# Optimization experiments

Hardware: AMD Instinct MI355X
Metric: run time of the kernel (lower is better)

## Reference

```python
import jax, jax.numpy as jnp
import numpy as np

V, D = 100000, 300
B, NCTX, NNEG = 16384, 10, 20


def setup_inputs() -> dict:
    key = jax.random.key(0)
    k1, k2, k3, k4, k5 = jax.random.split(key, 5)
    bound = 0.5 / D
    in_embed_w = jax.random.uniform(k1, (V, D), jnp.float32, -bound, bound)
    # torch init is zeros for out_embed; use small random values so the
    # negative-sampling math is numerically non-trivial for testing.
    out_embed_w = jax.random.normal(k2, (V, D), jnp.float32) * 0.01
    context_words = jax.random.randint(k3, (B, NCTX), 0, V)
    center_word = jax.random.randint(k4, (B,), 0, V)
    neg_words = jax.random.randint(k5, (B, NNEG), 0, V)
    return {
        "context_words": context_words,
        "center_word": center_word,
        "neg_words": neg_words,
        "in_embed_w": in_embed_w,
        "out_embed_w": out_embed_w,
    }


def reference(context_words, center_word, neg_words, in_embed_w, out_embed_w):
    # gather + mean-pool context embeddings: [B, 2w, D] -> [B, D]
    ctx_mean = jnp.mean(in_embed_w[context_words], axis=1)
    # positive score: dot(ctx_mean, out_embed[center])  -> [B]
    pos_emb = out_embed_w[center_word]                      # [B, D]
    pos_score = jnp.sum(ctx_mean * pos_emb, axis=1)         # [B]
    # negative scores: bmm([B, K, D], [B, D, 1]) -> [B, K]
    neg_emb = out_embed_w[neg_words]                        # [B, K, D]
    neg_score = jnp.einsum('bkd,bd->bk', neg_emb, ctx_mean)  # [B, K]
    loss = -jnp.mean(
        jax.nn.log_sigmoid(pos_score)
        + jnp.sum(jax.nn.log_sigmoid(-neg_score), axis=1)
    )
    return loss
```

## Files before the change

### kernel.cpp

```cpp
#include <hip/hip_runtime.h>
#include <math.h>

#define DIM    300
#define CH     75
#define NCTX   10
#define NNEG   20
#define NROWS  (1 + NNEG)
#define BLOCK  256
#define G      7

__device__ __forceinline__ float log_sigmoid(float x) {
    return fminf(x, 0.0f) - log1pf(expf(-fabsf(x)));
}
__device__ __forceinline__ float dot4(float4 a, float4 b) {
    return a.x * b.x + a.y * b.y + a.z * b.z + a.w * b.w;
}
__device__ __forceinline__ float4 add4(float4 a, float4 b) {
    return make_float4(a.x + b.x, a.y + b.y, a.z + b.z, a.w + b.w);
}

__global__ __launch_bounds__(BLOCK) void cbow_loss_kernel(
    const int*   __restrict__ ctx,
    const int*   __restrict__ center,
    const int*   __restrict__ neg,
    const float* __restrict__ in_w,
    const float* __restrict__ out_w,
    float*       __restrict__ out,
    int B, float inv_b)
{
    __shared__ float wsum[4];

    const int tid  = threadIdx.x;
    const int wave = tid >> 6;
    const int lane = tid & 63;
    const int b    = blockIdx.x * 4 + wave;

    float loss = 0.f;
    if (b < B) {
        int myidx = 0;
        if (lane < NCTX)                 myidx = ctx[b * NCTX + lane];
        else if (lane == NCTX)           myidx = center[b];
        else if (lane < NCTX + NROWS)    myidx = neg[b * NNEG + (lane - NCTX - 1)];

        const int   c1 = lane;
        const int   c2 = (64 + lane < CH) ? 64 + lane : CH - 1;
        const float w1 = (64 + lane < CH) ? 1.f : 0.f;

        float4 a0 = make_float4(0.f, 0.f, 0.f, 0.f);
        float4 a1 = make_float4(0.f, 0.f, 0.f, 0.f);
        #pragma unroll
        for (int j = 0; j < NCTX; ++j) {
            const int w = __shfl(myidx, j, 64);
            const float4* row = (const float4*)(in_w + (long long)w * DIM);
            a0 = add4(a0, row[c1]);
            a1 = add4(a1, row[c2]);
        }
        const float s0 = 1.f / NCTX;
        const float s1 = w1 / NCTX;
        const float4 m0 = make_float4(a0.x * s0, a0.y * s0, a0.z * s0, a0.w * s0);
        const float4 m1 = make_float4(a1.x * s1, a1.y * s1, a1.z * s1, a1.w * s1);

        #pragma unroll
        for (int t = 0; t < 3; ++t) {
            float4 r0[G], r1[G];
            #pragma unroll
            for (int k = 0; k < G; ++k) {
                const int w = __shfl(myidx, NCTX + t * G + k, 64);
                const float4* row = (const float4*)(out_w + (long long)w * DIM);
                r0[k] = row[c1];
                r1[k] = row[c2];
            }
            float p[G];
            #pragma unroll
            for (int k = 0; k < G; ++k)
                p[k] = dot4(r0[k], m0) + dot4(r1[k], m1);
            #pragma unroll
            for (int off = 32; off > 0; off >>= 1) {
                #pragma unroll
                for (int k = 0; k < G; ++k)
                    p[k] += __shfl_down(p[k], off, 64);
            }
            if (lane == 0) {
                #pragma unroll
                for (int k = 0; k < G; ++k) {
                    const int i = t * G + k;
                    loss += log_sigmoid(i == 0 ? p[k] : -p[k]);
                }
            }
        }
    }

    if (lane == 0) wsum[wave] = loss;
    __syncthreads();
    if (tid == 0)
        atomicAdd(out, -(wsum[0] + wsum[1] + wsum[2] + wsum[3]) * inv_b);
}

extern "C" void kernel_launch(void* const* d_in, const int* in_sizes, int n_in,
                              void* d_out, int out_size, void* d_ws, size_t ws_size,
                              hipStream_t stream) {
    const int*   ctx    = (const int*)  d_in[0];
    const int*   center = (const int*)  d_in[1];
    const int*   neg    = (const int*)  d_in[2];
    const float* in_w   = (const float*)d_in[3];
    const float* out_w  = (const float*)d_in[4];
    float*       out    = (float*)d_out;

    const int B = in_sizes[1];

    hipMemsetAsync(out, 0, sizeof(float), stream);
    cbow_loss_kernel<<<(B + 3) / 4, BLOCK, 0, stream>>>(ctx, center, neg,
                                                        in_w, out_w, out,
                                                        B, 1.0f / (float)B);
}
```

Baseline: 299.7 us.

## Use transpose-style butterfly reduction for 21 dot products and per-wave atomics

Replaces the per-row shfl_down reductions (21 rows × 6 steps) with a recursive-halving butterfly that splits the rows across lane halves at each xor step, so each lane ends up holding one completed dot product. The log-sigmoid is then evaluated in parallel across lanes with fast __expf/__logf intrinsics and summed with one more wave reduction. The LDS/syncthreads block reduction is dropped in favour of one atomicAdd per wave, which adds atomic contention and slightly reduces log precision. The intent is to cut shuffle count and serial lane-0 transcendental work in a kernel that is likely bound by gathered memory traffic.

```diff
diff --git a/kernel.cpp b/kernel.cpp
--- a/kernel.cpp
+++ b/kernel.cpp
@@ -9,8 +9,8 @@
 #define BLOCK  256
 #define G      7
 
-__device__ __forceinline__ float log_sigmoid(float x) {
-    return fminf(x, 0.0f) - log1pf(expf(-fabsf(x)));
+__device__ __forceinline__ float logsig_fast(float x) {
+    return fminf(x, 0.f) - __logf(1.f + __expf(-fabsf(x)));
 }
 __device__ __forceinline__ float dot4(float4 a, float4 b) {
     return a.x * b.x + a.y * b.y + a.z * b.z + a.w * b.w;
@@ -28,72 +28,92 @@
     float*       __restrict__ out,
     int B, float inv_b)
 {
-    __shared__ float wsum[4];
-
     const int tid  = threadIdx.x;
     const int wave = tid >> 6;
     const int lane = tid & 63;
     const int b    = blockIdx.x * 4 + wave;
+    if (b >= B) return;
 
-    float loss = 0.f;
-    if (b < B) {
-        int myidx = 0;
-        if (lane < NCTX)                 myidx = ctx[b * NCTX + lane];
-        else if (lane == NCTX)           myidx = center[b];
-        else if (lane < NCTX + NROWS)    myidx = neg[b * NNEG + (lane - NCTX - 1)];
+    int myidx = 0;
+    if (lane < NCTX)              myidx = ctx[b * NCTX + lane];
+    else if (lane == NCTX)        myidx = center[b];
+    else if (lane < NCTX + NROWS) myidx = neg[b * NNEG + (lane - NCTX - 1)];
 
-        const int   c1 = lane;
-        const int   c2 = (64 + lane < CH) ? 64 + lane : CH - 1;
-        const float w1 = (64 + lane < CH) ? 1.f : 0.f;
+    const int   c1 = lane;
+    const int   c2 = (64 + lane < CH) ? 64 + lane : CH - 1;
+    const float w1 = (64 + lane < CH) ? 1.f : 0.f;
 
-        float4 a0 = make_float4(0.f, 0.f, 0.f, 0.f);
-        float4 a1 = make_float4(0.f, 0.f, 0.f, 0.f);
+    float4 a0 = make_float4(0.f, 0.f, 0.f, 0.f);
+    float4 a1 = make_float4(0.f, 0.f, 0.f, 0.f);
+    #pragma unroll
+    for (int j = 0; j < NCTX; ++j) {
+        const int w = __shfl(myidx, j, 64);
+        const float4* row = (const float4*)(in_w + (long long)w * DIM);
+        a0 = add4(a0, row[c1]);
+        a1 = add4(a1, row[c2]);
+    }
+    const float s0 = 1.f / NCTX;
+    const float s1 = w1 / NCTX;
+    const float4 m0 = make_float4(a0.x * s0, a0.y * s0, a0.z * s0, a0.w * s0);
+    const float4 m1 = make_float4(a1.x * s1, a1.y * s1, a1.z * s1, a1.w * s1);
+
+    float p[NROWS];
+    #pragma unroll
+    for (int t = 0; t < 3; ++t) {
+        float4 r0[G], r1[G];
         #pragma unroll
-        for (int j = 0; j < NCTX; ++j) {
-            const int w = __shfl(myidx, j, 64);
-            const float4* row = (const float4*)(in_w + (long long)w * DIM);
-            a0 = add4(a0, row[c1]);
-            a1 = add4(a1, row[c2]);
+        for (int k = 0; k < G; ++k) {
+            const int w = __shfl(myidx, NCTX + t * G + k, 64);
+            const float4* row = (const float4*)(out_w + (long long)w * DIM);
+            r0[k] = row[c1];
+            r1[k] = row[c2];
         }
-        const float s0 = 1.f / NCTX;
-        const float s1 = w1 / NCTX;
-        const float4 m0 = make_float4(a0.x * s0, a0.y * s0, a0.z * s0, a0.w * s0);
-        const float4 m1 = make_float4(a1.x * s1, a1.y * s1, a1.z * s1, a1.w * s1);
-
         #pragma unroll
-        for (int t = 0; t < 3; ++t) {
-            float4 r0[G], r1[G];
-            #pragma unroll
-            for (int k = 0; k < G; ++k) {
-                const int w = __shfl(myidx, NCTX + t * G + k, 64);
-                const float4* row = (const float4*)(out_w + (long long)w * DIM);
-                r0[k] = row[c1];
-                r1[k] = row[c2];
-            }
-            float p[G];
-            #pragma unroll
-            for (int k = 0; k < G; ++k)
-                p[k] = dot4(r0[k], m0) + dot4(r1[k], m1);
-            #pragma unroll
-            for (int off = 32; off > 0; off >>= 1) {
-                #pragma unroll
-                for (int k = 0; k < G; ++k)
-                    p[k] += __shfl_down(p[k], off, 64);
-            }
-            if (lane == 0) {
-                #pragma unroll
-                for (int k = 0; k < G; ++k) {
-                    const int i = t * G + k;
-                    loss += log_sigmoid(i == 0 ? p[k] : -p[k]);
-                }
-            }
-        }
+        for (int k = 0; k < G; ++k)
+            p[t * G + k] = dot4(r0[k], m0) + dot4(r1[k], m1);
     }
 
-    if (lane == 0) wsum[wave] = loss;
-    __syncthreads();
-    if (tid == 0)
-        atomicAdd(out, -(wsum[0] + wsum[1] + wsum[2] + wsum[3]) * inv_b);
+    const bool B5 = lane & 32, B4 = lane & 16, B3 = lane & 8;
+    const bool B2 = lane & 4,  B1 = lane & 2,  B0 = lane & 1;
+
+    #pragma unroll
+    for (int k = 0; k < NROWS; ++k) p[k] += __shfl_xor(p[k], 32, 64);
+    float q[11];
+    #pragma unroll
+    for (int j = 0; j < 10; ++j) q[j] = B5 ? p[2 * j + 1] : p[2 * j];
+    q[10] = p[20];
+    #pragma unroll
+    for (int j = 0; j < 11; ++j) q[j] += __shfl_xor(q[j], 16, 64);
+    float r[6];
+    #pragma unroll
+    for (int i = 0; i < 5; ++i) r[i] = B4 ? q[2 * i + 1] : q[2 * i];
+    r[5] = q[10];
+    #pragma unroll
+    for (int i = 0; i < 6; ++i) r[i] += __shfl_xor(r[i], 8, 64);
+    float s[3];
+    #pragma unroll
+    for (int h = 0; h < 3; ++h) s[h] = B3 ? r[2 * h + 1] : r[2 * h];
+    #pragma unroll
+    for (int h = 0; h < 3; ++h) s[h] += __shfl_xor(s[h], 4, 64);
+    float t0 = B2 ? s[1] : s[0];
+    float t1 = s[2];
+    t0 += __shfl_xor(t0, 2, 64);
+    t1 += __shfl_xor(t1, 2, 64);
+    float u = B1 ? t1 : t0;
+    u += __shfl_xor(u, 1, 64);
+
+    int  k;
+    bool canon;
+    if (!B1)      { k = (B2 ? 8 : 0) + (B3 ? 4 : 0) + (B4 ? 2 : 0) + (B5 ? 1 : 0); canon = !B0; }
+    else if (!B3) { k = 16 + (B4 ? 2 : 0) + (B5 ? 1 : 0); canon = !B0 && !B2; }
+    else          { k = 20; canon = (lane == 10); }
+
+    float val = canon ? logsig_fast(k == 0 ? u : -u) : 0.f;
+    #pragma unroll
+    for (int off = 32; off > 0; off >>= 1)
+        val += __shfl_xor(val, off, 64);
+
+    if (lane == 0) atomicAdd(out, -val * inv_b);
 }
 
 extern "C" void kernel_launch(void* const* d_in, const int* in_sizes, int n_in,
```

Result: slower. 432.9 us (+44.4%).
